# Performance work log

Hardware: AMD Instinct MI355X
Metric: run time of the kernel (lower is better)

The kernel has to match this reference:

```python
import jax, jax.numpy as jnp
import numpy as np

# --- SOM geometry constants (match init_kwargs) ---
MAP_ROWS, MAP_COLS = 32, 32
N_PROTO = MAP_ROWS * MAP_COLS
SIGMA = 1.0
PBC = True


def _build_neighborhood():
    """Gaussian neighborhood h[i,j]=exp(-dist(i,j)^2/(2*sigma^2)) on a hexagonal
    grid with periodic boundary conditions (faithful to Neighborhoods(...,'Hexagons','grid',PBC=True))."""
    rr, cc = np.meshgrid(np.arange(MAP_ROWS), np.arange(MAP_COLS), indexing='ij')
    # hexagonal lattice coordinates: odd rows shifted by 0.5, row spacing sqrt(3)/2
    x = cc + 0.5 * (rr % 2)
    y = rr * (np.sqrt(3.0) / 2.0)
    pos = np.stack([x.ravel(), y.ravel()], axis=1).astype(np.float64)  # [M, 2]
    diff = pos[:, None, :] - pos[None, :, :]                            # [M, M, 2]
    if PBC:
        width = float(MAP_COLS)
        height = MAP_ROWS * (np.sqrt(3.0) / 2.0)
        d2 = np.full((N_PROTO, N_PROTO), np.inf)
        for sx in (-1.0, 0.0, 1.0):
            for sy in (-1.0, 0.0, 1.0):
                dx = diff[..., 0] + sx * width
                dy = diff[..., 1] + sy * height
                d2 = np.minimum(d2, dx * dx + dy * dy)
    else:
        d2 = (diff ** 2).sum(-1)
    return np.exp(-d2 / (2.0 * SIGMA ** 2)).astype(np.float32)         # [M, M]


H = jnp.asarray(_build_neighborhood())  # constant [M, M] neighborhood matrix


def setup_inputs() -> dict:
    key = jax.random.key(0)
    k1, k2 = jax.random.split(key)
    inputs = jax.random.normal(k1, (16384, 256), dtype=jnp.float32)
    prototypes = jax.random.normal(k2, (N_PROTO, 256), dtype=jnp.float32) * 0.05
    return {"inputs": inputs, "prototypes": prototypes}


def reference(inputs, prototypes):
    # squared euclidean distances d[n, m] = ||x_n - p_m||^2, computed without
    # materializing the (N, M, D) broadcast intermediate
    x2 = jnp.sum(inputs * inputs, axis=1, keepdims=True)        # [N, 1]
    p2 = jnp.sum(prototypes * prototypes, axis=1)               # [M]
    d = x2 - 2.0 * (inputs @ prototypes.T) + p2[None, :]        # [N, M]
    energies = H @ d.T                                          # [M, N]
    bmus = jnp.argmin(energies, axis=0)                         # [N]
    out = 0.5 * jnp.take_along_axis(energies, bmus[None, :], axis=0)  # [1, N]
    return out
```

## Files before the change

### kernel.cpp

```cpp
#include <hip/hip_runtime.h>
#include <hip/hip_bf16.h>
#include <math.h>

#define D 256
#define NPROTO 1024
#define NROWS 16384
#define WRr 13
#define WCc 18
#define WJ (WRr * WCc)
#define JSUB 59
#define GMAT_BLOCKS (NPROTO / 4)

typedef __attribute__((ext_vector_type(8))) short short8;
typedef __attribute__((ext_vector_type(4))) float f32x4;

__device__ __forceinline__ short f2bf(float f) {
    union { __hip_bfloat16 b; short s; } u;
    u.b = __float2bfloat16(f);
    return u.s;
}

__device__ __forceinline__ void gload_lds16(void* lds, const void* g) {
    __builtin_amdgcn_global_load_lds(
        (const __attribute__((address_space(1))) unsigned*)g,
        (__attribute__((address_space(3))) unsigned*)lds, 16, 0, 0);
}

__device__ __forceinline__ void proto_pos(int idx, double& x, double& y) {
    int r = idx >> 5, c = idx & 31;
    x = (double)c + 0.5 * (double)(r & 1);
    y = (double)r * 0.86602540378443864676;
}

__device__ __forceinline__ float hval(int i, int j) {
    double xi, yi, xj, yj;
    proto_pos(i, xi, yi);
    proto_pos(j, xj, yj);
    double dx0 = xi - xj, dy0 = yi - yj;
    const double W = 32.0;
    const double Hh = 27.712812921102035;
    double best = 1e300;
#pragma unroll
    for (int sx = -1; sx <= 1; ++sx) {
        double dx = dx0 + (double)sx * W;
#pragma unroll
        for (int sy = -1; sy <= 1; ++sy) {
            double dy = dy0 + (double)sy * Hh;
            double d2 = dx * dx + dy * dy;
            best = fmin(best, d2);
        }
    }
    return (float)exp(-0.5 * best);
}


__global__ void __launch_bounds__(256) prep_kernel(
    const float* __restrict__ P, short* __restrict__ GbS,
    float* __restrict__ hsum, float* __restrict__ hp2,
    unsigned* __restrict__ out) {
    __shared__ float ht[4][WJ];
    __shared__ int jrow[WJ];
    __shared__ __align__(16) float gpart[4][4][256];
    __shared__ float hqred[4][4];
    __shared__ float hsred[4][4];
    int t = threadIdx.x;
    int bx = blockIdx.x;

    if (t < 64) out[bx * 64 + t] = 0x7f800000u;

    int i0 = bx * 4;
    int r0 = i0 >> 5, c0 = i0 & 31;

    for (int u = t; u < WJ; u += 256) {
        int jr = (r0 + (u / WCc) - 6 + 32) & 31;
        int jc = (c0 + (u % WCc) - 7 + 32) & 31;
        int j = jr * 32 + jc;
        jrow[u] = j;
#pragma unroll
        for (int s = 0; s < 4; ++s) ht[s][u] = hval(i0 + s, j);
    }
    __syncthreads();

    int w = t >> 6, lane = t & 63;
    int j0 = w * JSUB;
    int j1 = (j0 + JSUB < WJ) ? j0 + JSUB : WJ;
    f32x4 g[4] = {{0.f, 0.f, 0.f, 0.f}, {0.f, 0.f, 0.f, 0.f},
                  {0.f, 0.f, 0.f, 0.f}, {0.f, 0.f, 0.f, 0.f}};
    float hqp[4] = {0.f, 0.f, 0.f, 0.f};
    float hsp[4] = {0.f, 0.f, 0.f, 0.f};
    for (int u = j0; u < j1; ++u) {
        f32x4 pv = *reinterpret_cast<const f32x4*>(P + (size_t)jrow[u] * D + lane * 4);
        float q = pv[0] * pv[0] + pv[1] * pv[1] + pv[2] * pv[2] + pv[3] * pv[3];
#pragma unroll
        for (int s = 0; s < 4; ++s) {
            float h = ht[s][u];
            g[s][0] = fmaf(h, pv[0], g[s][0]);
            g[s][1] = fmaf(h, pv[1], g[s][1]);
            g[s][2] = fmaf(h, pv[2], g[s][2]);
            g[s][3] = fmaf(h, pv[3], g[s][3]);
            hqp[s] = fmaf(h, q, hqp[s]);
            hsp[s] += h;
        }
    }
#pragma unroll
    for (int s = 0; s < 4; ++s)
        *reinterpret_cast<f32x4*>(&gpart[w][s][lane * 4]) = g[s];
#pragma unroll
    for (int s = 0; s < 4; ++s) {
#pragma unroll
        for (int off = 1; off < 64; off <<= 1) hqp[s] += __shfl_xor(hqp[s], off);
    }
    if (lane == 0) {
#pragma unroll
        for (int s = 0; s < 4; ++s) { hqred[w][s] = hqp[s]; hsred[w][s] = hsp[s]; }
    }
    __syncthreads();

    {
        int s = t >> 6;
        f32x4 gs = *reinterpret_cast<const f32x4*>(&gpart[0][s][lane * 4]);
#pragma unroll
        for (int ww = 1; ww < 4; ++ww) {
            f32x4 gp = *reinterpret_cast<const f32x4*>(&gpart[ww][s][lane * 4]);
            gs[0] += gp[0]; gs[1] += gp[1]; gs[2] += gp[2]; gs[3] += gp[3];
        }
        float h0 = __shfl_down(gs[0], 1);
        float h1 = __shfl_down(gs[1], 1);
        float h2 = __shfl_down(gs[2], 1);
        float h3 = __shfl_down(gs[3], 1);
        if (!(lane & 1)) {
            int c = lane >> 1;
            int kt = c >> 2;
            int slot = c & 3;
            int i = i0 + s;
            int key = (i & 3) ^ ((i >> 2) & 3);
            short8 wv;
            wv[0] = f2bf(gs[0]); wv[1] = f2bf(gs[1]); wv[2] = f2bf(gs[2]); wv[3] = f2bf(gs[3]);
            wv[4] = f2bf(h0);    wv[5] = f2bf(h1);    wv[6] = f2bf(h2);    wv[7] = f2bf(h3);
            *reinterpret_cast<short8*>(
                GbS + (size_t)kt * (NPROTO * 32) + (size_t)i * 32 +
                ((slot ^ key) << 3)) = wv;
        }
    }
    if (t < 4) {
        hsum[i0 + t] = hsred[0][t] + hsred[1][t] + hsred[2][t] + hsred[3][t];
    } else if (t < 8) {
        int s = t - 4;
        hp2[i0 + s] = hqred[0][s] + hqred[1][s] + hqred[2][s] + hqred[3][s];
    }
}

__global__ void __launch_bounds__(256, 2) som12_kernel(
    const float* __restrict__ X, const short* __restrict__ GbS,
    const float* __restrict__ hsum, const float* __restrict__ hp2,
    unsigned* __restrict__ out) {
    __shared__ __align__(16) float Xsf[2][128 * 32];
    __shared__ __align__(16) short Gs[2][128 * 32];
    __shared__ float x2s[128];
    __shared__ float red[2][128];

    const int t = threadIdx.x;
    const int lane = t & 63;
    const int wid = t >> 6;
    const int wr = wid >> 1;
    const int wc = wid & 1;
    const int lm = lane & 15;
    const int lq = lane >> 4;
    const int keyG = (lm & 3) ^ ((lm >> 2) & 3);
    const int k8 = lm & 7;

    const int bx = blockIdx.x;
    const int w1024 = ((bx & 7) << 7) | (bx >> 3);
    const int n0 = (w1024 >> 3) * 128;
    const int ib0 = (w1024 & 7) * 128;

    const int srow = t >> 1;
    const int sh_ = t & 1;
    const int skey = srow & 7;

    f32x4 acc[4][4];
#pragma unroll
    for (int m = 0; m < 4; ++m)
#pragma unroll
        for (int n = 0; n < 4; ++n) acc[m][n] = (f32x4){0.f, 0.f, 0.f, 0.f};

    float sq = 0.f;
    f32x4 xr0, xr1, xr2, xr3;

    auto issueX = [&](int kt) {
        const f32x4* src = reinterpret_cast<const f32x4*>(
            X + (size_t)(n0 + srow) * D + kt * 32 + sh_ * 16);
        xr0 = src[0]; xr1 = src[1]; xr2 = src[2]; xr3 = src[3];
    };
    auto issueG = [&](int b, int kt) {
#pragma unroll
        for (int q = 0; q < 2; ++q)
            gload_lds16((char*)(&Gs[b][0]) + q * 4096 + t * 16,
                        GbS + (size_t)kt * (NPROTO * 32) +
                        (size_t)(ib0 + q * 64 + (t >> 2)) * 32 + ((t & 3) << 3));
    };
    auto writeX = [&](int b) {
        char* base = (char*)(&Xsf[b][0]) + srow * 128;
        *reinterpret_cast<f32x4*>(base + (((sh_ * 4 + 0) ^ skey) << 4)) = xr0;
        *reinterpret_cast<f32x4*>(base + (((sh_ * 4 + 1) ^ skey) << 4)) = xr1;
        *reinterpret_cast<f32x4*>(base + (((sh_ * 4 + 2) ^ skey) << 4)) = xr2;
        *reinterpret_cast<f32x4*>(base + (((sh_ * 4 + 3) ^ skey) << 4)) = xr3;
        sq += xr0[0] * xr0[0] + xr0[1] * xr0[1] + xr0[2] * xr0[2] + xr0[3] * xr0[3] +
              xr1[0] * xr1[0] + xr1[1] * xr1[1] + xr1[2] * xr1[2] + xr1[3] * xr1[3] +
              xr2[0] * xr2[0] + xr2[1] * xr2[1] + xr2[2] * xr2[2] + xr2[3] * xr2[3] +
              xr3[0] * xr3[0] + xr3[1] * xr3[1] + xr3[2] * xr3[2] + xr3[3] * xr3[3];
    };

    auto compute = [&](int b) {
        const char* xbase = (const char*)(&Xsf[b][0]);
        const short* gb = &Gs[b][0];
        short8 a[4];
#pragma unroll
        for (int m = 0; m < 4; ++m) {
            int row = wr * 64 + m * 16 + lm;
            const char* rb = xbase + row * 128;
            f32x4 lo = *reinterpret_cast<const f32x4*>(rb + ((((lq * 2) + 0) ^ k8) << 4));
            f32x4 hi = *reinterpret_cast<const f32x4*>(rb + ((((lq * 2) + 1) ^ k8) << 4));
            short8 av;
            av[0] = f2bf(lo[0]); av[1] = f2bf(lo[1]); av[2] = f2bf(lo[2]); av[3] = f2bf(lo[3]);
            av[4] = f2bf(hi[0]); av[5] = f2bf(hi[1]); av[6] = f2bf(hi[2]); av[7] = f2bf(hi[3]);
            a[m] = av;
        }
        short8 b_[4];
#pragma unroll
        for (int n = 0; n < 4; ++n)
            b_[n] = *reinterpret_cast<const short8*>(
                &gb[(wc * 64 + n * 16 + lm) * 32 + ((lq ^ keyG) << 3)]);
        __builtin_amdgcn_s_setprio(1);
#pragma unroll
        for (int m = 0; m < 4; ++m)
#pragma unroll
            for (int n = 0; n < 4; ++n)
                acc[m][n] = __builtin_amdgcn_mfma_f32_16x16x32_bf16(a[m], b_[n], acc[m][n], 0, 0, 0);
        __builtin_amdgcn_s_setprio(0);
    };

    issueG(0, 0);
    issueX(0);
    writeX(0);
    __syncthreads();

#pragma unroll
    for (int kt = 0; kt < 8; ++kt) {
        if (kt < 7) {
            issueG((kt + 1) & 1, kt + 1);
            issueX(kt + 1);
        }
        compute(kt & 1);
        if (kt < 7) writeX((kt + 1) & 1);
        __syncthreads();
    }

    if (sh_ == 0) x2s[srow] = sq;
    __syncthreads();
    if (sh_ == 1) x2s[srow] += sq;
    __syncthreads();

    float x2v[4][4];
#pragma unroll
    for (int m = 0; m < 4; ++m)
#pragma unroll
        for (int j = 0; j < 4; ++j)
            x2v[m][j] = x2s[wr * 64 + m * 16 + lq * 4 + j];

    float rmin[4][4];
#pragma unroll
    for (int m = 0; m < 4; ++m)
#pragma unroll
        for (int j = 0; j < 4; ++j) rmin[m][j] = 3.4e38f;

#pragma unroll
    for (int ni = 0; ni < 4; ++ni) {
        int ig = ib0 + wc * 64 + ni * 16 + lm;
        float hs = hsum[ig];
        float hq = hp2[ig];
#pragma unroll
        for (int m = 0; m < 4; ++m)
#pragma unroll
            for (int j = 0; j < 4; ++j) {
                float e = fmaf(hs, x2v[m][j], hq) - 2.0f * acc[m][ni][j];
                rmin[m][j] = fminf(rmin[m][j], e);
            }
    }

#pragma unroll
    for (int m = 0; m < 4; ++m)
#pragma unroll
        for (int j = 0; j < 4; ++j) {
            float v = rmin[m][j];
            v = fminf(v, __shfl_xor(v, 1));
            v = fminf(v, __shfl_xor(v, 2));
            v = fminf(v, __shfl_xor(v, 4));
            v = fminf(v, __shfl_xor(v, 8));
            rmin[m][j] = v;
        }
    if (lm == 0) {
#pragma unroll
        for (int m = 0; m < 4; ++m)
#pragma unroll
            for (int j = 0; j < 4; ++j)
                red[wc][wr * 64 + m * 16 + lq * 4 + j] = rmin[m][j];
    }
    __syncthreads();
    if (t < 128) {
        float v = fminf(red[0][t], red[1][t]);
        atomicMin(out + n0 + t, __float_as_uint(0.5f * v));
    }
}

extern "C" void kernel_launch(void* const* d_in, const int* in_sizes, int n_in,
                              void* d_out, int out_size, void* d_ws, size_t ws_size,
                              hipStream_t stream) {
    const float* X = (const float*)d_in[0];
    const float* P = (const float*)d_in[1];
    unsigned* out = (unsigned*)d_out;
    (void)in_sizes; (void)n_in; (void)out_size; (void)ws_size;

    float* ws = (float*)d_ws;
    float* hsum = ws + 1024;
    float* hp2 = ws + 2048;
    short* GbS = (short*)(ws + 32768);

    prep_kernel<<<GMAT_BLOCKS, 256, 0, stream>>>(P, GbS, hsum, hp2, out);
    som12_kernel<<<1024, 256, 0, stream>>>(X, GbS, hsum, hp2, out);
}
```

Measured before the change: 36.93 us.

## Store X tile as bf16 in LDS, raise occupancy, use float neighborhood math

The main kernel now converts X to bf16 once, when it writes the tile to shared memory, instead of keeping fp32 in LDS and converting on every fragment read. This halves the X tile's LDS footprint and removes the repeated conversions from the MFMA loop. Launch bounds go from 2 to 4 blocks per CU to use the freed LDS. The prep kernel's hexagonal neighborhood weights switch from double precision with exp to float with __expf, which is cheaper but slightly less accurate and could change tie-breaking in the argmin.

```diff
diff --git a/kernel.cpp b/kernel.cpp
--- a/kernel.cpp
+++ b/kernel.cpp
@@ -14,6 +14,10 @@
 typedef __attribute__((ext_vector_type(8))) short short8;
 typedef __attribute__((ext_vector_type(4))) float f32x4;
 
+__device__ __forceinline__ int swz_key(int row) {
+    return (row & 3) ^ ((row >> 2) & 3);
+}
+
 __device__ __forceinline__ short f2bf(float f) {
     union { __hip_bfloat16 b; short s; } u;
     u.b = __float2bfloat16(f);
@@ -26,31 +30,28 @@
         (__attribute__((address_space(3))) unsigned*)lds, 16, 0, 0);
 }
 
-__device__ __forceinline__ void proto_pos(int idx, double& x, double& y) {
-    int r = idx >> 5, c = idx & 31;
-    x = (double)c + 0.5 * (double)(r & 1);
-    y = (double)r * 0.86602540378443864676;
-}
-
 __device__ __forceinline__ float hval(int i, int j) {
-    double xi, yi, xj, yj;
-    proto_pos(i, xi, yi);
-    proto_pos(j, xj, yj);
-    double dx0 = xi - xj, dy0 = yi - yj;
-    const double W = 32.0;
-    const double Hh = 27.712812921102035;
-    double best = 1e300;
+    int ri = i >> 5, ci = i & 31;
+    int rj = j >> 5, cj = j & 31;
+    float xi = (float)ci + 0.5f * (float)(ri & 1);
+    float yi = (float)ri * 0.86602540f;
+    float xj = (float)cj + 0.5f * (float)(rj & 1);
+    float yj = (float)rj * 0.86602540f;
+    float dx0 = xi - xj, dy0 = yi - yj;
+    const float W = 32.0f;
+    const float Hh = 27.7128129f;
+    float best = 3.4e38f;
 #pragma unroll
     for (int sx = -1; sx <= 1; ++sx) {
-        double dx = dx0 + (double)sx * W;
+        float dx = dx0 + (float)sx * W;
 #pragma unroll
         for (int sy = -1; sy <= 1; ++sy) {
-            double dy = dy0 + (double)sy * Hh;
-            double d2 = dx * dx + dy * dy;
-            best = fmin(best, d2);
-        }
-    }
-    return (float)exp(-0.5 * best);
+            float dy = dy0 + (float)sy * Hh;
+            float d2 = dx * dx + dy * dy;
+            best = fminf(best, d2);
+        }
+    }
+    return __expf(-0.5f * best);
 }
 
 
@@ -133,13 +134,12 @@
             int kt = c >> 2;
             int slot = c & 3;
             int i = i0 + s;
-            int key = (i & 3) ^ ((i >> 2) & 3);
             short8 wv;
             wv[0] = f2bf(gs[0]); wv[1] = f2bf(gs[1]); wv[2] = f2bf(gs[2]); wv[3] = f2bf(gs[3]);
             wv[4] = f2bf(h0);    wv[5] = f2bf(h1);    wv[6] = f2bf(h2);    wv[7] = f2bf(h3);
             *reinterpret_cast<short8*>(
                 GbS + (size_t)kt * (NPROTO * 32) + (size_t)i * 32 +
-                ((slot ^ key) << 3)) = wv;
+                ((slot ^ swz_key(i)) << 3)) = wv;
         }
     }
     if (t < 4) {
@@ -150,11 +150,11 @@
     }
 }
 
-__global__ void __launch_bounds__(256, 2) som12_kernel(
+__global__ void __launch_bounds__(256, 4) som14_kernel(
     const float* __restrict__ X, const short* __restrict__ GbS,
     const float* __restrict__ hsum, const float* __restrict__ hp2,
     unsigned* __restrict__ out) {
-    __shared__ __align__(16) float Xsf[2][128 * 32];
+    __shared__ __align__(16) short Xs[2][128 * 32];
     __shared__ __align__(16) short Gs[2][128 * 32];
     __shared__ float x2s[128];
     __shared__ float red[2][128];
@@ -166,8 +166,7 @@
     const int wc = wid & 1;
     const int lm = lane & 15;
     const int lq = lane >> 4;
-    const int keyG = (lm & 3) ^ ((lm >> 2) & 3);
-    const int k8 = lm & 7;
+    const int key = (lm & 3) ^ ((lm >> 2) & 3);
 
     const int bx = blockIdx.x;
     const int w1024 = ((bx & 7) << 7) | (bx >> 3);
@@ -176,7 +175,7 @@
 
     const int srow = t >> 1;
     const int sh_ = t & 1;
-    const int skey = srow & 7;
+    const int skey = swz_key(srow);
 
     f32x4 acc[4][4];
 #pragma unroll
@@ -200,11 +199,14 @@
                         (size_t)(ib0 + q * 64 + (t >> 2)) * 32 + ((t & 3) << 3));
     };
     auto writeX = [&](int b) {
-        char* base = (char*)(&Xsf[b][0]) + srow * 128;
-        *reinterpret_cast<f32x4*>(base + (((sh_ * 4 + 0) ^ skey) << 4)) = xr0;
-        *reinterpret_cast<f32x4*>(base + (((sh_ * 4 + 1) ^ skey) << 4)) = xr1;
-        *reinterpret_cast<f32x4*>(base + (((sh_ * 4 + 2) ^ skey) << 4)) = xr2;
-        *reinterpret_cast<f32x4*>(base + (((sh_ * 4 + 3) ^ skey) << 4)) = xr3;
+        short8 w0, w1;
+        w0[0] = f2bf(xr0[0]); w0[1] = f2bf(xr0[1]); w0[2] = f2bf(xr0[2]); w0[3] = f2bf(xr0[3]);
+        w0[4] = f2bf(xr1[0]); w0[5] = f2bf(xr1[1]); w0[6] = f2bf(xr1[2]); w0[7] = f2bf(xr1[3]);
+        w1[0] = f2bf(xr2[0]); w1[1] = f2bf(xr2[1]); w1[2] = f2bf(xr2[2]); w1[3] = f2bf(xr2[3]);
+        w1[4] = f2bf(xr3[0]); w1[5] = f2bf(xr3[1]); w1[6] = f2bf(xr3[2]); w1[7] = f2bf(xr3[3]);
+        char* base = (char*)(&Xs[b][0]) + srow * 64;
+        *reinterpret_cast<short8*>(base + (((sh_ * 2 + 0) ^ skey) << 4)) = w0;
+        *reinterpret_cast<short8*>(base + (((sh_ * 2 + 1) ^ skey) << 4)) = w1;
         sq += xr0[0] * xr0[0] + xr0[1] * xr0[1] + xr0[2] * xr0[2] + xr0[3] * xr0[3] +
               xr1[0] * xr1[0] + xr1[1] * xr1[1] + xr1[2] * xr1[2] + xr1[3] * xr1[3] +
               xr2[0] * xr2[0] + xr2[1] * xr2[1] + xr2[2] * xr2[2] + xr2[3] * xr2[3] +
@@ -212,31 +214,22 @@
     };
 
     auto compute = [&](int b) {
-        const char* xbase = (const char*)(&Xsf[b][0]);
+        const short* xb = &Xs[b][0];
         const short* gb = &Gs[b][0];
-        short8 a[4];
-#pragma unroll
-        for (int m = 0; m < 4; ++m) {
-            int row = wr * 64 + m * 16 + lm;
-            const char* rb = xbase + row * 128;
-            f32x4 lo = *reinterpret_cast<const f32x4*>(rb + ((((lq * 2) + 0) ^ k8) << 4));
-            f32x4 hi = *reinterpret_cast<const f32x4*>(rb + ((((lq * 2) + 1) ^ k8) << 4));
-            short8 av;
-            av[0] = f2bf(lo[0]); av[1] = f2bf(lo[1]); av[2] = f2bf(lo[2]); av[3] = f2bf(lo[3]);
-            av[4] = f2bf(hi[0]); av[5] = f2bf(hi[1]); av[6] = f2bf(hi[2]); av[7] = f2bf(hi[3]);
-            a[m] = av;
-        }
-        short8 b_[4];
+        const int so = (lq ^ key) << 3;
+        short8 a[4], bb[4];
+#pragma unroll
+        for (int m = 0; m < 4; ++m)
+            a[m] = *reinterpret_cast<const short8*>(&xb[(wr * 64 + m * 16 + lm) * 32 + so]);
 #pragma unroll
         for (int n = 0; n < 4; ++n)
-            b_[n] = *reinterpret_cast<const short8*>(
-                &gb[(wc * 64 + n * 16 + lm) * 32 + ((lq ^ keyG) << 3)]);
+            bb[n] = *reinterpret_cast<const short8*>(&gb[(wc * 64 + n * 16 + lm) * 32 + so]);
         __builtin_amdgcn_s_setprio(1);
 #pragma unroll
         for (int m = 0; m < 4; ++m)
 #pragma unroll
             for (int n = 0; n < 4; ++n)
-                acc[m][n] = __builtin_amdgcn_mfma_f32_16x16x32_bf16(a[m], b_[n], acc[m][n], 0, 0, 0);
+                acc[m][n] = __builtin_amdgcn_mfma_f32_16x16x32_bf16(a[m], bb[n], acc[m][n], 0, 0, 0);
         __builtin_amdgcn_s_setprio(0);
     };
 
@@ -327,5 +320,5 @@
     short* GbS = (short*)(ws + 32768);
 
     prep_kernel<<<GMAT_BLOCKS, 256, 0, stream>>>(P, GbS, hsum, hp2, out);
-    som12_kernel<<<1024, 256, 0, stream>>>(X, GbS, hsum, hp2, out);
-}
+    som14_kernel<<<1024, 256, 0, stream>>>(X, GbS, hsum, hp2, out);
+}
```

Result: slower. 39.93 us (+8.1%).
